# Optimization experiments

Measured on AMD Instinct MI355X. Metric: run time of the kernel, lower is better.

The kernel has to match this reference:

```python
import jax, jax.numpy as jnp
import numpy as np

N, M, F, B = 100000, 12, 64, 41  # atoms, max neighbors, atom feat dim, bond feat dim
EPS = 1e-5


def setup_inputs() -> dict:
    key = jax.random.key(0)
    ks = jax.random.split(key, 8)
    neighbor_indices = jax.random.randint(ks[0], (N, M), 0, N, dtype=jnp.int32)
    atom_features = jax.random.normal(ks[1], (N, F), dtype=jnp.float32)
    bond_features = jax.random.normal(ks[2], (N, M, B), dtype=jnp.float32)
    W = jax.random.normal(ks[3], (2 * F + B, 2 * F), dtype=jnp.float32) * 0.05
    b = jnp.zeros((2 * F,), dtype=jnp.float32)
    bn1_scale = 1.0 + 0.02 * jax.random.normal(ks[4], (2 * F,), dtype=jnp.float32)
    bn1_offset = 0.02 * jax.random.normal(ks[5], (2 * F,), dtype=jnp.float32)
    bn2_scale = 1.0 + 0.02 * jax.random.normal(ks[6], (F,), dtype=jnp.float32)
    bn2_offset = 0.02 * jax.random.normal(ks[7], (F,), dtype=jnp.float32)
    return {"neighbor_indices": neighbor_indices, "atom_features": atom_features,
            "bond_features": bond_features, "W": W, "b": b,
            "bn1_scale": bn1_scale, "bn1_offset": bn1_offset,
            "bn2_scale": bn2_scale, "bn2_offset": bn2_offset}


def batchnorm(x, scale, offset):
    # haiku BatchNorm, training mode: batch stats over all axes but channel (last)
    mean = jnp.mean(x, axis=0, keepdims=True)
    var = jnp.mean(jnp.square(x), axis=0, keepdims=True) - jnp.square(mean)
    inv = scale * jax.lax.rsqrt(var + EPS)
    return (x - mean) * inv + offset


def reference(neighbor_indices, atom_features, bond_features, W, b,
              bn1_scale, bn1_offset, bn2_scale, bn2_offset):
    n = atom_features.shape[0]
    nbr_feats = atom_features[neighbor_indices]  # (N, M, F) gather
    self_feats = jnp.broadcast_to(atom_features[:, None, :], (n, M, F))
    total = jnp.concatenate([self_feats, nbr_feats, bond_features], axis=2)  # (N, M, 2F+B)
    gated = total @ W + b  # (N, M, 2F)
    gated = batchnorm(gated.reshape(-1, 2 * F), bn1_scale, bn1_offset).reshape(n, M, 2 * F)
    nbr_filter, nbr_core = jnp.split(gated, 2, axis=2)
    summed = jnp.sum(jax.nn.sigmoid(nbr_filter) * jax.nn.softplus(nbr_core), axis=1)  # (N, F)
    summed = batchnorm(summed, bn2_scale, bn2_offset)
    return jax.nn.softplus(atom_features + summed)
```

## Files before the change

### kernel.cpp

```cpp
#include <hip/hip_runtime.h>
#include <hip/hip_bf16.h>
#include <math.h>


#define NATOMS  100000
#define MNBR    12
#define FDIM    64
#define BDIM    41
#define C2F     128
#define EPSBN   1e-5f
#define NBLK    2048
#define GROUPS  (NATOMS/4)
#define AR      136
#define PR      72

typedef __attribute__((ext_vector_type(8))) short  short8;
typedef __attribute__((ext_vector_type(4))) float  f32x4;

__device__ __forceinline__ float softplusf(float x) {
    return fmaxf(x, 0.f) + __logf(1.f + __expf(-fabsf(x)));
}
__device__ __forceinline__ float sigmoidf(float x) {
    return 1.f / (1.f + __expf(-x));
}
__device__ __forceinline__ unsigned short f2bf(float f) {
    unsigned int x = __builtin_bit_cast(unsigned int, f);
    unsigned int r = (x + 0x7fff + ((x >> 16) & 1)) >> 16;
    return (unsigned short)r;
}
__device__ __forceinline__ unsigned int pkbf(float a, float b) {
    unsigned short lo = __builtin_bit_cast(unsigned short, __float2bfloat16(a));
    unsigned short hi = __builtin_bit_cast(unsigned short, __float2bfloat16(b));
    return (unsigned)lo | ((unsigned)hi << 16);
}
__device__ __forceinline__ float bflo(unsigned int u) {
    return __builtin_bit_cast(float, u << 16);
}
__device__ __forceinline__ float bfhi(unsigned int u) {
    return __builtin_bit_cast(float, u & 0xffff0000u);
}
__device__ __forceinline__ float bf2f(unsigned short u) {
    return __builtin_bit_cast(float, ((unsigned int)u) << 16);
}

__global__ __launch_bounds__(256) void k_pack(
    const float* __restrict__ W,
    unsigned short* __restrict__ Wsn, unsigned short* __restrict__ Wpk)
{
    const int t0 = blockIdx.x*256 + threadIdx.x;
    for (int idx = t0; idx < 8*2*64*8; idx += gridDim.x*256) {
        int e = idx & 7, lane = (idx >> 3) & 63, ks = (idx >> 9) & 1, n = idx >> 10;
        int k   = ks*32 + (lane >> 4)*8 + e;
        int col = n*16 + (lane & 15);
        Wsn[idx] = f2bf(W[k*C2F + col]);
    }
    for (int idx = t0; idx < 8*4*64*8; idx += gridDim.x*256) {
        int e = idx & 7, lane = (idx >> 3) & 63, ks = (idx >> 9) & 3, n = idx >> 11;
        int k   = ks*32 + (lane >> 4)*8 + e;
        int col = n*16 + (lane & 15);
        float v = (k < 105) ? W[(64 + k)*C2F + col] : 0.f;
        Wpk[idx] = f2bf(v);
    }
}

__global__ __launch_bounds__(256, 4) void k_proj(
    const float* __restrict__ atomF, const unsigned short* __restrict__ Wsn,
    unsigned short* __restrict__ PselfBf)
{
    __shared__ __align__(16) unsigned short A[64*PR];
    const int tid = threadIdx.x, w = tid >> 6, lane = tid & 63;
    const int g = lane >> 4, x = lane & 15;
    short8 B0[2], B1[2];
    #pragma unroll
    for (int ks = 0; ks < 2; ++ks) {
        B0[ks] = *(const short8*)(Wsn + ((w*2 + ks)*64 + lane)*8);
        B1[ks] = *(const short8*)(Wsn + (((w+4)*2 + ks)*64 + lane)*8);
    }
    for (int a0 = blockIdx.x*64; a0 < NATOMS; a0 += gridDim.x*64) {
        __syncthreads();
        #pragma unroll
        for (int it = 0; it < 4; ++it) {
            int idx = it*256 + tid;
            int p = idx >> 4, c = idx & 15;
            int i = a0 + p;
            float4 v = make_float4(0.f, 0.f, 0.f, 0.f);
            if (i < NATOMS) v = *(const float4*)(atomF + (size_t)i*FDIM + 4*c);
            uint2 u; u.x = pkbf(v.x, v.y); u.y = pkbf(v.z, v.w);
            *(uint2*)(A + p*PR + 4*c) = u;
        }
        __syncthreads();
        f32x4 z = {0.f, 0.f, 0.f, 0.f};
        f32x4 acc[4][2];
        #pragma unroll
        for (int m = 0; m < 4; ++m) { acc[m][0] = z; acc[m][1] = z; }
        #pragma unroll
        for (int ks = 0; ks < 2; ++ks) {
            #pragma unroll
            for (int m = 0; m < 4; ++m) {
                short8 a = *(const short8*)(A + (m*16 + x)*PR + ks*32 + g*8);
                acc[m][0] = __builtin_amdgcn_mfma_f32_16x16x32_bf16(a, B0[ks], acc[m][0], 0, 0, 0);
                acc[m][1] = __builtin_amdgcn_mfma_f32_16x16x32_bf16(a, B1[ks], acc[m][1], 0, 0, 0);
            }
        }
        #pragma unroll
        for (int m = 0; m < 4; ++m) {
            int i = a0 + m*16 + g*4;
            #pragma unroll
            for (int rg = 0; rg < 4; ++rg) {
                if (i + rg < NATOMS) {
                    PselfBf[(size_t)(i+rg)*C2F + w*16 + x]     = f2bf(acc[m][0][rg]);
                    PselfBf[(size_t)(i+rg)*C2F + (w+4)*16 + x] = f2bf(acc[m][1][rg]);
                }
            }
        }
    }
}

__global__ __launch_bounds__(256, 4) void k_gemm(
    const int* __restrict__ nbr, const float* __restrict__ atomF,
    const float* __restrict__ bond, const unsigned short* __restrict__ Wpk,
    const unsigned short* __restrict__ PselfBf,
    uint4* __restrict__ gated, float* __restrict__ partial1)
{
    __shared__ __align__(16) unsigned short A[48*AR];
    __shared__ int Ni[48];
    const int tid = threadIdx.x, w = tid >> 6, lane = tid & 63;
    const int g = lane >> 4, x = lane & 15;
    const int ch0 = w*16 + x;
    short8 B0[4], B1[4];
    #pragma unroll
    for (int ks = 0; ks < 4; ++ks) {
        B0[ks] = *(const short8*)(Wpk + ((w*4 + ks)*64 + lane)*8);
        B1[ks] = *(const short8*)(Wpk + (((w+4)*4 + ks)*64 + lane)*8);
    }
    for (int idx = tid; idx < 48*AR/2; idx += 256) ((unsigned int*)A)[idx] = 0u;
    float s0 = 0.f, q0 = 0.f, s1 = 0.f, q1 = 0.f;

    for (int grp = blockIdx.x; grp < GROUPS; grp += gridDim.x) {
        const int base = grp*4;
        __syncthreads();
        if (tid < 48) Ni[tid] = nbr[base*MNBR + tid];
        __syncthreads();
        #pragma unroll
        for (int it = 0; it < 6; ++it) {
            int idx = it*256 + tid;
            int p = idx >> 5, c = idx & 31;
            if (c < 16) {
                int r = Ni[p];
                float4 v = *(const float4*)(atomF + (size_t)r*FDIM + 4*c);
                uint2 u; u.x = pkbf(v.x, v.y); u.y = pkbf(v.z, v.w);
                *(uint2*)(A + p*AR + 4*c) = u;
            } else if (c < 27) {
                int cc = c - 16;
                int pa = p/12;
                const float* bp = bond + (size_t)(base + pa)*(MNBR*BDIM)
                                       + (p - pa*12)*BDIM + 4*cc;
                float b0 = bp[0], b1 = 0.f, b2 = 0.f, b3 = 0.f;
                if (cc < 10) { b1 = bp[1]; b2 = bp[2]; b3 = bp[3]; }
                uint2 u; u.x = pkbf(b0, b1); u.y = pkbf(b2, b3);
                *(uint2*)(A + p*AR + 64 + 4*cc) = u;
            }
        }
        __syncthreads();
        f32x4 z = {0.f, 0.f, 0.f, 0.f};
        f32x4 acc[3][2];
        #pragma unroll
        for (int m = 0; m < 3; ++m) { acc[m][0] = z; acc[m][1] = z; }
        #pragma unroll
        for (int ks = 0; ks < 4; ++ks) {
            #pragma unroll
            for (int m = 0; m < 3; ++m) {
                short8 a = *(const short8*)(A + (m*16 + x)*AR + ks*32 + g*8);
                acc[m][0] = __builtin_amdgcn_mfma_f32_16x16x32_bf16(a, B0[ks], acc[m][0], 0, 0, 0);
                acc[m][1] = __builtin_amdgcn_mfma_f32_16x16x32_bf16(a, B1[ks], acc[m][1], 0, 0, 0);
            }
        }
        uint4* gbase = gated + ((size_t)grp*4 + w)*3*64 + lane;
        #pragma unroll
        for (int m = 0; m < 3; ++m) {
            int ia = base + (m*16 + g*4)/12;
            float ps0 = bf2f(PselfBf[(size_t)ia*C2F + ch0]);
            float ps1 = bf2f(PselfBf[(size_t)ia*C2F + 64 + ch0]);
            float v00 = acc[m][0][0] + ps0, v01 = acc[m][0][1] + ps0;
            float v02 = acc[m][0][2] + ps0, v03 = acc[m][0][3] + ps0;
            float v10 = acc[m][1][0] + ps1, v11 = acc[m][1][1] + ps1;
            float v12 = acc[m][1][2] + ps1, v13 = acc[m][1][3] + ps1;
            s0 += (v00 + v01) + (v02 + v03);
            s1 += (v10 + v11) + (v12 + v13);
            q0 = fmaf(v00, v00, q0); q0 = fmaf(v01, v01, q0);
            q0 = fmaf(v02, v02, q0); q0 = fmaf(v03, v03, q0);
            q1 = fmaf(v10, v10, q1); q1 = fmaf(v11, v11, q1);
            q1 = fmaf(v12, v12, q1); q1 = fmaf(v13, v13, q1);
            uint4 pk;
            pk.x = pkbf(v00, v01); pk.y = pkbf(v02, v03);
            pk.z = pkbf(v10, v11); pk.w = pkbf(v12, v13);
            gbase[m*64] = pk;
        }
    }
    s0 += __shfl_xor(s0, 16); s0 += __shfl_xor(s0, 32);
    s1 += __shfl_xor(s1, 16); s1 += __shfl_xor(s1, 32);
    q0 += __shfl_xor(q0, 16); q0 += __shfl_xor(q0, 32);
    q1 += __shfl_xor(q1, 16); q1 += __shfl_xor(q1, 32);
    if (g == 0) {
        float* pb = partial1 + blockIdx.x*256;
        pb[ch0]            = s0; pb[64 + ch0]        = s1;
        pb[C2F + ch0]      = q0; pb[C2F + 64 + ch0]  = q1;
    }
}

__global__ __launch_bounds__(256) void k_red(
    const float* __restrict__ in, float* __restrict__ outp, int width)
{
    const int b = blockIdx.x;
    for (int c = threadIdx.x; c < width; c += 256) {
        float s = 0.f;
        #pragma unroll 4
        for (int k = 0; k < 16; ++k) s += in[(size_t)(b*16 + k)*width + c];
        outp[(size_t)b*width + c] = s;
    }
}

__global__ __launch_bounds__(1024) void k_bn1_finalize(
    const float* __restrict__ red1, const float* __restrict__ scale,
    const float* __restrict__ offset, float* __restrict__ prm1)
{
    __shared__ float redS[1024], redQ[1024];
    const int tid = threadIdx.x, c = tid & 127, h = tid >> 7;
    float S = 0.f, Q = 0.f;
    for (int blk = h; blk < 128; blk += 8) {
        S += red1[blk*256 + c];
        Q += red1[blk*256 + 128 + c];
    }
    redS[tid] = S; redQ[tid] = Q;
    __syncthreads();
    if (tid < 128) {
        float Sa = 0.f, Qa = 0.f;
        #pragma unroll
        for (int hh = 0; hh < 8; ++hh) { Sa += redS[hh*128 + c]; Qa += redQ[hh*128 + c]; }
        const float invn = 1.f / (float)(NATOMS * MNBR);
        float mean = Sa * invn;
        float var  = Qa * invn - mean*mean;
        float inv  = scale[c] * rsqrtf(var + EPSBN);
        prm1[c]       = inv;
        prm1[128 + c] = offset[c] - mean*inv;
    }
}

__global__ __launch_bounds__(256, 8) void k_apply(
    const uint4* __restrict__ gated, const float* __restrict__ prm1,
    float* __restrict__ summed, float* __restrict__ partial2)
{
    __shared__ float Y[12*66];
    __shared__ float red[256];
    const int tid = threadIdx.x, w = tid >> 6, lane = tid & 63;
    const int g = lane >> 4, x = lane & 15;
    const int ch0 = w*16 + x;
    const float iv0 = prm1[ch0],      of0 = prm1[C2F + ch0];
    const float iv1 = prm1[64 + ch0], of1 = prm1[C2F + 64 + ch0];
    float s2 = 0.f, q2 = 0.f;

    for (int grp = blockIdx.x; grp < GROUPS; grp += gridDim.x) {
        __syncthreads();
        const uint4* gbase = gated + ((size_t)grp*4 + w)*3*64 + lane;
        #pragma unroll
        for (int m = 0; m < 3; ++m) {
            uint4 pk = gbase[m*64];
            float y00 = bflo(pk.x)*iv0 + of0, y01 = bfhi(pk.x)*iv0 + of0;
            float y02 = bflo(pk.y)*iv0 + of0, y03 = bfhi(pk.y)*iv0 + of0;
            float y10 = bflo(pk.z)*iv1 + of1, y11 = bfhi(pk.z)*iv1 + of1;
            float y12 = bflo(pk.w)*iv1 + of1, y13 = bfhi(pk.w)*iv1 + of1;
            float sY = sigmoidf(y00)*softplusf(y10) + sigmoidf(y01)*softplusf(y11)
                     + sigmoidf(y02)*softplusf(y12) + sigmoidf(y03)*softplusf(y13);
            Y[(m*4 + g)*66 + ch0] = sY;
        }
        __syncthreads();
        float sv = Y[(3*w)*66 + lane] + Y[(3*w + 1)*66 + lane] + Y[(3*w + 2)*66 + lane];
        summed[(size_t)(grp*4 + w)*FDIM + lane] = sv;
        s2 += sv; q2 = fmaf(sv, sv, q2);
    }
    red[tid] = s2; __syncthreads();
    if (tid < 64) partial2[blockIdx.x*128 + tid]
        = red[tid] + red[tid+64] + red[tid+128] + red[tid+192];
    __syncthreads();
    red[tid] = q2; __syncthreads();
    if (tid < 64) partial2[blockIdx.x*128 + 64 + tid]
        = red[tid] + red[tid+64] + red[tid+128] + red[tid+192];
}

__global__ __launch_bounds__(1024) void k_bn2_finalize(
    const float* __restrict__ red2, const float* __restrict__ scale,
    const float* __restrict__ offset, float* __restrict__ prm2)
{
    __shared__ float redS[1024], redQ[1024];
    const int tid = threadIdx.x, f = tid & 63, h = tid >> 6;
    float S = 0.f, Q = 0.f;
    for (int blk = h; blk < 128; blk += 16) {
        S += red2[blk*128 + f];
        Q += red2[blk*128 + 64 + f];
    }
    redS[tid] = S; redQ[tid] = Q;
    __syncthreads();
    if (tid < 64) {
        float Sa = 0.f, Qa = 0.f;
        #pragma unroll
        for (int hh = 0; hh < 16; ++hh) { Sa += redS[hh*64 + f]; Qa += redQ[hh*64 + f]; }
        const float invn = 1.f / (float)NATOMS;
        float mean = Sa * invn;
        float var  = Qa * invn - mean*mean;
        float inv  = scale[f] * rsqrtf(var + EPSBN);
        prm2[f]      = inv;
        prm2[64 + f] = offset[f] - mean*inv;
    }
}

__global__ __launch_bounds__(256) void k_final(
    const float* __restrict__ atomF, const float* __restrict__ summed,
    const float* __restrict__ prm2, float* __restrict__ out)
{
    __shared__ float iv[64], of[64];
    if (threadIdx.x < 64) {
        iv[threadIdx.x] = prm2[threadIdx.x];
        of[threadIdx.x] = prm2[64 + threadIdx.x];
    }
    __syncthreads();
    const int total4 = NATOMS*FDIM/4;
    for (int t = blockIdx.x*blockDim.x + threadIdx.x; t < total4;
         t += gridDim.x*blockDim.x) {
        float4 a = ((const float4*)atomF)[t];
        float4 s = ((const float4*)summed)[t];
        int fb = (t*4) & 63;
        float4 r;
        r.x = softplusf(a.x + s.x*iv[fb]   + of[fb]);
        r.y = softplusf(a.y + s.y*iv[fb+1] + of[fb+1]);
        r.z = softplusf(a.z + s.z*iv[fb+2] + of[fb+2]);
        r.w = softplusf(a.w + s.w*iv[fb+3] + of[fb+3]);
        ((float4*)out)[t] = r;
    }
}

extern "C" void kernel_launch(void* const* d_in, const int* in_sizes, int n_in,
                              void* d_out, int out_size, void* d_ws, size_t ws_size,
                              hipStream_t stream)
{
    const int*   nbr   = (const int*)  d_in[0];
    const float* atomF = (const float*)d_in[1];
    const float* bond  = (const float*)d_in[2];
    const float* W     = (const float*)d_in[3];
    const float* s1    = (const float*)d_in[5];
    const float* o1    = (const float*)d_in[6];
    const float* s2    = (const float*)d_in[7];
    const float* o2    = (const float*)d_in[8];
    float* out = (float*)d_out;

    uint4* gated        = (uint4*)d_ws;
    unsigned short* PselfBf = (unsigned short*)(gated + (size_t)GROUPS*12*64);
    float* summed   = (float*)(PselfBf + (size_t)NATOMS*C2F);
    float* partial1 = summed   + (size_t)NATOMS*FDIM;
    float* partial2 = partial1 + (size_t)NBLK*256;
    float* red1     = partial2 + (size_t)NBLK*128;
    float* red2     = red1     + 128*256;
    float* prm1     = red2     + 128*128;
    float* prm2     = prm1     + 256;
    unsigned short* Wsn = (unsigned short*)(prm2 + 128);
    unsigned short* Wpk = Wsn + 8192;

    hipLaunchKernelGGL(k_pack,         dim3(64),   dim3(256),  0, stream, W, Wsn, Wpk);
    hipLaunchKernelGGL(k_proj,         dim3(782),  dim3(256),  0, stream, atomF, Wsn, PselfBf);
    hipLaunchKernelGGL(k_gemm,         dim3(NBLK), dim3(256),  0, stream,
                       nbr, atomF, bond, Wpk, PselfBf, gated, partial1);
    hipLaunchKernelGGL(k_red,          dim3(128),  dim3(256),  0, stream, partial1, red1, 256);
    hipLaunchKernelGGL(k_bn1_finalize, dim3(1),    dim3(1024), 0, stream, red1, s1, o1, prm1);
    hipLaunchKernelGGL(k_apply,        dim3(NBLK), dim3(256),  0, stream,
                       gated, prm1, summed, partial2);
    hipLaunchKernelGGL(k_red,          dim3(128),  dim3(256),  0, stream, partial2, red2, 128);
    hipLaunchKernelGGL(k_bn2_finalize, dim3(1),    dim3(1024), 0, stream, red2, s2, o2, prm2);
    hipLaunchKernelGGL(k_final,        dim3(2048), dim3(256),  0, stream, atomF, summed, prm2, out);
}
```

Baseline: 397.3 us.

## Double-buffer neighbor tile loads and gather from a bf16 atom copy

k_proj now also writes a bf16 copy of the atom features, and k_gemm gathers neighbor rows from that copy, which halves the gather bytes. k_gemm's shared tile is double-buffered: the next group's gather and bond loads are issued into registers before the MFMA work on the current group and written to the alternate buffer afterward, which hides load latency. The Ni shared array and one barrier per iteration are dropped. The cost is extra registers for staging, twice the LDS, and an additional 12.8MB write in k_proj.

After: 394.2 us. No clear change (-0.8%).

```diff
diff --git a/kernel.cpp b/kernel.cpp
--- a/kernel.cpp
+++ b/kernel.cpp
@@ -65,7 +65,7 @@
 
 __global__ __launch_bounds__(256, 4) void k_proj(
     const float* __restrict__ atomF, const unsigned short* __restrict__ Wsn,
-    unsigned short* __restrict__ PselfBf)
+    unsigned short* __restrict__ PselfBf, unsigned short* __restrict__ atomBf)
 {
     __shared__ __align__(16) unsigned short A[64*PR];
     const int tid = threadIdx.x, w = tid >> 6, lane = tid & 63;
@@ -87,6 +87,7 @@
             if (i < NATOMS) v = *(const float4*)(atomF + (size_t)i*FDIM + 4*c);
             uint2 u; u.x = pkbf(v.x, v.y); u.y = pkbf(v.z, v.w);
             *(uint2*)(A + p*PR + 4*c) = u;
+            if (i < NATOMS) *(uint2*)(atomBf + (size_t)i*FDIM + 4*c) = u;
         }
         __syncthreads();
         f32x4 z = {0.f, 0.f, 0.f, 0.f};
@@ -117,13 +118,12 @@
 }
 
 __global__ __launch_bounds__(256, 4) void k_gemm(
-    const int* __restrict__ nbr, const float* __restrict__ atomF,
+    const int* __restrict__ nbr, const unsigned short* __restrict__ atomBf,
     const float* __restrict__ bond, const unsigned short* __restrict__ Wpk,
     const unsigned short* __restrict__ PselfBf,
     uint4* __restrict__ gated, float* __restrict__ partial1)
 {
-    __shared__ __align__(16) unsigned short A[48*AR];
-    __shared__ int Ni[48];
+    __shared__ __align__(16) unsigned short A[2][48*AR];
     const int tid = threadIdx.x, w = tid >> 6, lane = tid & 63;
     const int g = lane >> 4, x = lane & 15;
     const int ch0 = w*16 + x;
@@ -133,35 +133,47 @@
         B0[ks] = *(const short8*)(Wpk + ((w*4 + ks)*64 + lane)*8);
         B1[ks] = *(const short8*)(Wpk + (((w+4)*4 + ks)*64 + lane)*8);
     }
-    for (int idx = tid; idx < 48*AR/2; idx += 256) ((unsigned int*)A)[idx] = 0u;
+    for (int idx = tid; idx < 2*48*AR/2; idx += 256) ((unsigned int*)A)[idx] = 0u;
+
+    uint2 st[6];
     float s0 = 0.f, q0 = 0.f, s1 = 0.f, q1 = 0.f;
 
-    for (int grp = blockIdx.x; grp < GROUPS; grp += gridDim.x) {
-        const int base = grp*4;
-        __syncthreads();
-        if (tid < 48) Ni[tid] = nbr[base*MNBR + tid];
-        __syncthreads();
-        #pragma unroll
-        for (int it = 0; it < 6; ++it) {
-            int idx = it*256 + tid;
-            int p = idx >> 5, c = idx & 31;
-            if (c < 16) {
-                int r = Ni[p];
-                float4 v = *(const float4*)(atomF + (size_t)r*FDIM + 4*c);
-                uint2 u; u.x = pkbf(v.x, v.y); u.y = pkbf(v.z, v.w);
-                *(uint2*)(A + p*AR + 4*c) = u;
-            } else if (c < 27) {
-                int cc = c - 16;
-                int pa = p/12;
-                const float* bp = bond + (size_t)(base + pa)*(MNBR*BDIM)
-                                       + (p - pa*12)*BDIM + 4*cc;
-                float b0 = bp[0], b1 = 0.f, b2 = 0.f, b3 = 0.f;
-                if (cc < 10) { b1 = bp[1]; b2 = bp[2]; b3 = bp[3]; }
-                uint2 u; u.x = pkbf(b0, b1); u.y = pkbf(b2, b3);
-                *(uint2*)(A + p*AR + 64 + 4*cc) = u;
-            }
-        }
-        __syncthreads();
+#define LOADG(GRP)                                                            \
+    {   const int base_ = (GRP)*4;                                            \
+        _Pragma("unroll")                                                     \
+        for (int it = 0; it < 6; ++it) {                                      \
+            int idx = it*256 + tid;                                           \
+            int p = idx >> 5, c = idx & 31;                                   \
+            if (c < 16) {                                                     \
+                int r = nbr[base_*MNBR + p];                                  \
+                st[it] = *(const uint2*)(atomBf + ((size_t)r << 6) + 4*c);    \
+            } else if (c < 27) {                                              \
+                int cc = c - 16;                                              \
+                int pa = p/12;                                                \
+                const float* bp = bond + (size_t)(base_ + pa)*(MNBR*BDIM)     \
+                                       + (p - pa*12)*BDIM + 4*cc;             \
+                float b0 = bp[0], b1 = 0.f, b2 = 0.f, b3 = 0.f;               \
+                if (cc < 10) { b1 = bp[1]; b2 = bp[2]; b3 = bp[3]; }          \
+                st[it].x = pkbf(b0, b1); st[it].y = pkbf(b2, b3);             \
+            }                                                                 \
+        } }
+
+#define WRITEA(BUF)                                                           \
+    {   _Pragma("unroll")                                                     \
+        for (int it = 0; it < 6; ++it) {                                      \
+            int idx = it*256 + tid;                                           \
+            int p = idx >> 5, c = idx & 31;                                   \
+            if (c < 16)      *(uint2*)(&A[BUF][p*AR + 4*c]) = st[it];         \
+            else if (c < 27) *(uint2*)(&A[BUF][p*AR + 64 + 4*(c-16)]) = st[it]; \
+        } }
+
+    int grp = blockIdx.x;
+    int cur = 0;
+    if (grp < GROUPS) { LOADG(grp); WRITEA(0); }
+    for (; grp < GROUPS; grp += gridDim.x) {
+        const int nxt = grp + gridDim.x;
+        __syncthreads();
+        if (nxt < GROUPS) LOADG(nxt);
         f32x4 z = {0.f, 0.f, 0.f, 0.f};
         f32x4 acc[3][2];
         #pragma unroll
@@ -170,11 +182,12 @@
         for (int ks = 0; ks < 4; ++ks) {
             #pragma unroll
             for (int m = 0; m < 3; ++m) {
-                short8 a = *(const short8*)(A + (m*16 + x)*AR + ks*32 + g*8);
+                short8 a = *(const short8*)(&A[cur][(m*16 + x)*AR + ks*32 + g*8]);
                 acc[m][0] = __builtin_amdgcn_mfma_f32_16x16x32_bf16(a, B0[ks], acc[m][0], 0, 0, 0);
                 acc[m][1] = __builtin_amdgcn_mfma_f32_16x16x32_bf16(a, B1[ks], acc[m][1], 0, 0, 0);
             }
         }
+        const int base = grp*4;
         uint4* gbase = gated + ((size_t)grp*4 + w)*3*64 + lane;
         #pragma unroll
         for (int m = 0; m < 3; ++m) {
@@ -196,7 +209,11 @@
             pk.z = pkbf(v10, v11); pk.w = pkbf(v12, v13);
             gbase[m*64] = pk;
         }
-    }
+        if (nxt < GROUPS) WRITEA(cur ^ 1);
+        cur ^= 1;
+    }
+#undef LOADG
+#undef WRITEA
     s0 += __shfl_xor(s0, 16); s0 += __shfl_xor(s0, 32);
     s1 += __shfl_xor(s1, 16); s1 += __shfl_xor(s1, 32);
     q0 += __shfl_xor(q0, 16); q0 += __shfl_xor(q0, 32);
@@ -354,7 +371,8 @@
 
     uint4* gated        = (uint4*)d_ws;
     unsigned short* PselfBf = (unsigned short*)(gated + (size_t)GROUPS*12*64);
-    float* summed   = (float*)(PselfBf + (size_t)NATOMS*C2F);
+    unsigned short* atomBf  = PselfBf + (size_t)NATOMS*C2F;
+    float* summed   = (float*)(atomBf + (size_t)NATOMS*FDIM);
     float* partial1 = summed   + (size_t)NATOMS*FDIM;
     float* partial2 = partial1 + (size_t)NBLK*256;
     float* red1     = partial2 + (size_t)NBLK*128;
@@ -365,9 +383,10 @@
     unsigned short* Wpk = Wsn + 8192;
 
     hipLaunchKernelGGL(k_pack,         dim3(64),   dim3(256),  0, stream, W, Wsn, Wpk);
-    hipLaunchKernelGGL(k_proj,         dim3(782),  dim3(256),  0, stream, atomF, Wsn, PselfBf);
+    hipLaunchKernelGGL(k_proj,         dim3(782),  dim3(256),  0, stream,
+                       atomF, Wsn, PselfBf, atomBf);
     hipLaunchKernelGGL(k_gemm,         dim3(NBLK), dim3(256),  0, stream,
-                       nbr, atomF, bond, Wpk, PselfBf, gated, partial1);
+                       nbr, atomBf, bond, Wpk, PselfBf, gated, partial1);
     hipLaunchKernelGGL(k_red,          dim3(128),  dim3(256),  0, stream, partial1, red1, 256);
     hipLaunchKernelGGL(k_bn1_finalize, dim3(1),    dim3(1024), 0, stream, red1, s1, o1, prm1);
     hipLaunchKernelGGL(k_apply,        dim3(NBLK), dim3(256),  0, stream,
```

## Precompute neighbor projection per atom and gather projected rows instead of features

Applied to the files above, without the earlier changes.

The neighbor-feature part of the matmul is now computed once per atom in the projection kernel (atomF @ W_nbr, stored as bf16), alongside the self projection. The main kernel then only runs the bond-feature matmul (K reduced from 128 to 64) and adds gathered rows of the precomputed neighbor projection in its epilogue. This drops the per-edge gather-and-convert of 64 floats into shared memory and halves the MFMA work. In exchange, each gathered row is 128 bf16 values instead of 64 floats, projection output doubles in size, and the neighbor term gets an extra bf16 rounding. Occupancy hint raised to 6 and LDS row stride shrunk.

Result: slower. 492.4 us (+24.0%).

```diff
diff --git a/kernel.cpp b/kernel.cpp
--- a/kernel.cpp
+++ b/kernel.cpp
@@ -11,7 +11,7 @@
 #define EPSBN   1e-5f
 #define NBLK    2048
 #define GROUPS  (NATOMS/4)
-#define AR      136
+#define AR      72
 #define PR      72
 
 typedef __attribute__((ext_vector_type(8))) short  short8;
@@ -45,36 +45,39 @@
 
 __global__ __launch_bounds__(256) void k_pack(
     const float* __restrict__ W,
-    unsigned short* __restrict__ Wsn, unsigned short* __restrict__ Wpk)
+    unsigned short* __restrict__ Wal, unsigned short* __restrict__ Wbd)
 {
     const int t0 = blockIdx.x*256 + threadIdx.x;
+    for (int idx = t0; idx < 2*8*2*64*8; idx += gridDim.x*256) {
+        int e = idx & 7, lane = (idx >> 3) & 63, ks = (idx >> 9) & 1;
+        int n = (idx >> 10) & 7, h = idx >> 13;
+        int k   = h*64 + ks*32 + (lane >> 4)*8 + e;
+        int col = n*16 + (lane & 15);
+        Wal[idx] = f2bf(W[k*C2F + col]);
+    }
     for (int idx = t0; idx < 8*2*64*8; idx += gridDim.x*256) {
         int e = idx & 7, lane = (idx >> 3) & 63, ks = (idx >> 9) & 1, n = idx >> 10;
-        int k   = ks*32 + (lane >> 4)*8 + e;
+        int kk  = ks*32 + (lane >> 4)*8 + e;
         int col = n*16 + (lane & 15);
-        Wsn[idx] = f2bf(W[k*C2F + col]);
-    }
-    for (int idx = t0; idx < 8*4*64*8; idx += gridDim.x*256) {
-        int e = idx & 7, lane = (idx >> 3) & 63, ks = (idx >> 9) & 3, n = idx >> 11;
-        int k   = ks*32 + (lane >> 4)*8 + e;
-        int col = n*16 + (lane & 15);
-        float v = (k < 105) ? W[(64 + k)*C2F + col] : 0.f;
-        Wpk[idx] = f2bf(v);
+        float v = (kk < BDIM) ? W[(2*FDIM + kk)*C2F + col] : 0.f;
+        Wbd[idx] = f2bf(v);
     }
 }
 
 __global__ __launch_bounds__(256, 4) void k_proj(
-    const float* __restrict__ atomF, const unsigned short* __restrict__ Wsn,
-    unsigned short* __restrict__ PselfBf)
+    const float* __restrict__ atomF, const unsigned short* __restrict__ Wal,
+    unsigned short* __restrict__ PselfBf, unsigned short* __restrict__ PnbrBf)
 {
     __shared__ __align__(16) unsigned short A[64*PR];
     const int tid = threadIdx.x, w = tid >> 6, lane = tid & 63;
     const int g = lane >> 4, x = lane & 15;
-    short8 B0[2], B1[2];
+    short8 Bs0[2], Bs1[2], Bn0[2], Bn1[2];
     #pragma unroll
     for (int ks = 0; ks < 2; ++ks) {
-        B0[ks] = *(const short8*)(Wsn + ((w*2 + ks)*64 + lane)*8);
-        B1[ks] = *(const short8*)(Wsn + (((w+4)*2 + ks)*64 + lane)*8);
+        Bs0[ks] = *(const short8*)(Wal + (((0*8 + w    )*2 + ks)*64 + lane)*8);
+        Bs1[ks] = *(const short8*)(Wal + (((0*8 + w + 4)*2 + ks)*64 + lane)*8);
+        Bn0[ks] = *(const short8*)(Wal + (((1*8 + w    )*2 + ks)*64 + lane)*8);
+        Bn1[ks] = *(const short8*)(Wal + (((1*8 + w + 4)*2 + ks)*64 + lane)*8);
     }
     for (int a0 = blockIdx.x*64; a0 < NATOMS; a0 += gridDim.x*64) {
         __syncthreads();
@@ -90,16 +93,19 @@
         }
         __syncthreads();
         f32x4 z = {0.f, 0.f, 0.f, 0.f};
-        f32x4 acc[4][2];
-        #pragma unroll
-        for (int m = 0; m < 4; ++m) { acc[m][0] = z; acc[m][1] = z; }
+        f32x4 acc[4][4];
+        #pragma unroll
+        for (int m = 0; m < 4; ++m)
+            { acc[m][0] = z; acc[m][1] = z; acc[m][2] = z; acc[m][3] = z; }
         #pragma unroll
         for (int ks = 0; ks < 2; ++ks) {
             #pragma unroll
             for (int m = 0; m < 4; ++m) {
                 short8 a = *(const short8*)(A + (m*16 + x)*PR + ks*32 + g*8);
-                acc[m][0] = __builtin_amdgcn_mfma_f32_16x16x32_bf16(a, B0[ks], acc[m][0], 0, 0, 0);
-                acc[m][1] = __builtin_amdgcn_mfma_f32_16x16x32_bf16(a, B1[ks], acc[m][1], 0, 0, 0);
+                acc[m][0] = __builtin_amdgcn_mfma_f32_16x16x32_bf16(a, Bs0[ks], acc[m][0], 0, 0, 0);
+                acc[m][1] = __builtin_amdgcn_mfma_f32_16x16x32_bf16(a, Bs1[ks], acc[m][1], 0, 0, 0);
+                acc[m][2] = __builtin_amdgcn_mfma_f32_16x16x32_bf16(a, Bn0[ks], acc[m][2], 0, 0, 0);
+                acc[m][3] = __builtin_amdgcn_mfma_f32_16x16x32_bf16(a, Bn1[ks], acc[m][3], 0, 0, 0);
             }
         }
         #pragma unroll
@@ -108,30 +114,33 @@
             #pragma unroll
             for (int rg = 0; rg < 4; ++rg) {
                 if (i + rg < NATOMS) {
-                    PselfBf[(size_t)(i+rg)*C2F + w*16 + x]     = f2bf(acc[m][0][rg]);
-                    PselfBf[(size_t)(i+rg)*C2F + (w+4)*16 + x] = f2bf(acc[m][1][rg]);
+                    size_t o = (size_t)(i+rg)*C2F;
+                    PselfBf[o + w*16 + x]       = f2bf(acc[m][0][rg]);
+                    PselfBf[o + (w+4)*16 + x]   = f2bf(acc[m][1][rg]);
+                    PnbrBf [o + w*16 + x]       = f2bf(acc[m][2][rg]);
+                    PnbrBf [o + (w+4)*16 + x]   = f2bf(acc[m][3][rg]);
                 }
             }
         }
     }
 }
 
-__global__ __launch_bounds__(256, 4) void k_gemm(
-    const int* __restrict__ nbr, const float* __restrict__ atomF,
-    const float* __restrict__ bond, const unsigned short* __restrict__ Wpk,
+__global__ __launch_bounds__(256, 6) void k_gemm2(
+    const int* __restrict__ nbr, const float* __restrict__ bond,
+    const unsigned short* __restrict__ Wbd,
     const unsigned short* __restrict__ PselfBf,
+    const unsigned short* __restrict__ PnbrBf,
     uint4* __restrict__ gated, float* __restrict__ partial1)
 {
     __shared__ __align__(16) unsigned short A[48*AR];
-    __shared__ int Ni[48];
     const int tid = threadIdx.x, w = tid >> 6, lane = tid & 63;
     const int g = lane >> 4, x = lane & 15;
     const int ch0 = w*16 + x;
-    short8 B0[4], B1[4];
+    short8 B0[2], B1[2];
     #pragma unroll
-    for (int ks = 0; ks < 4; ++ks) {
-        B0[ks] = *(const short8*)(Wpk + ((w*4 + ks)*64 + lane)*8);
-        B1[ks] = *(const short8*)(Wpk + (((w+4)*4 + ks)*64 + lane)*8);
+    for (int ks = 0; ks < 2; ++ks) {
+        B0[ks] = *(const short8*)(Wbd + ((w*2 + ks)*64 + lane)*8);
+        B1[ks] = *(const short8*)(Wbd + (((w+4)*2 + ks)*64 + lane)*8);
     }
     for (int idx = tid; idx < 48*AR/2; idx += 256) ((unsigned int*)A)[idx] = 0u;
     float s0 = 0.f, q0 = 0.f, s1 = 0.f, q1 = 0.f;
@@ -139,26 +148,25 @@
     for (int grp = blockIdx.x; grp < GROUPS; grp += gridDim.x) {
         const int base = grp*4;
         __syncthreads();
-        if (tid < 48) Ni[tid] = nbr[base*MNBR + tid];
-        __syncthreads();
-        #pragma unroll
-        for (int it = 0; it < 6; ++it) {
+        int4 ridx[3];
+        float ps0[3], ps1[3];
+        #pragma unroll
+        for (int m = 0; m < 3; ++m) {
+            ridx[m] = *(const int4*)(nbr + base*MNBR + m*16 + g*4);
+            int ia = base + (m*16 + g*4)/12;
+            ps0[m] = bf2f(PselfBf[(size_t)ia*C2F + ch0]);
+            ps1[m] = bf2f(PselfBf[(size_t)ia*C2F + 64 + ch0]);
+        }
+        #pragma unroll
+        for (int it = 0; it < 3; ++it) {
             int idx = it*256 + tid;
-            int p = idx >> 5, c = idx & 31;
-            if (c < 16) {
-                int r = Ni[p];
-                float4 v = *(const float4*)(atomF + (size_t)r*FDIM + 4*c);
-                uint2 u; u.x = pkbf(v.x, v.y); u.y = pkbf(v.z, v.w);
-                *(uint2*)(A + p*AR + 4*c) = u;
-            } else if (c < 27) {
-                int cc = c - 16;
-                int pa = p/12;
-                const float* bp = bond + (size_t)(base + pa)*(MNBR*BDIM)
-                                       + (p - pa*12)*BDIM + 4*cc;
+            int p = idx >> 4, c = idx & 15;
+            if (c < 11) {
+                const float* bp = bond + (size_t)base*(MNBR*BDIM) + p*BDIM + 4*c;
                 float b0 = bp[0], b1 = 0.f, b2 = 0.f, b3 = 0.f;
-                if (cc < 10) { b1 = bp[1]; b2 = bp[2]; b3 = bp[3]; }
+                if (c < 10) { b1 = bp[1]; b2 = bp[2]; b3 = bp[3]; }
                 uint2 u; u.x = pkbf(b0, b1); u.y = pkbf(b2, b3);
-                *(uint2*)(A + p*AR + 64 + 4*cc) = u;
+                *(uint2*)(&A[p*AR + 4*c]) = u;
             }
         }
         __syncthreads();
@@ -167,10 +175,10 @@
         #pragma unroll
         for (int m = 0; m < 3; ++m) { acc[m][0] = z; acc[m][1] = z; }
         #pragma unroll
-        for (int ks = 0; ks < 4; ++ks) {
+        for (int ks = 0; ks < 2; ++ks) {
             #pragma unroll
             for (int m = 0; m < 3; ++m) {
-                short8 a = *(const short8*)(A + (m*16 + x)*AR + ks*32 + g*8);
+                short8 a = *(const short8*)(&A[(m*16 + x)*AR + ks*32 + g*8]);
                 acc[m][0] = __builtin_amdgcn_mfma_f32_16x16x32_bf16(a, B0[ks], acc[m][0], 0, 0, 0);
                 acc[m][1] = __builtin_amdgcn_mfma_f32_16x16x32_bf16(a, B1[ks], acc[m][1], 0, 0, 0);
             }
@@ -178,22 +186,19 @@
         uint4* gbase = gated + ((size_t)grp*4 + w)*3*64 + lane;
         #pragma unroll
         for (int m = 0; m < 3; ++m) {
-            int ia = base + (m*16 + g*4)/12;
-            float ps0 = bf2f(PselfBf[(size_t)ia*C2F + ch0]);
-            float ps1 = bf2f(PselfBf[(size_t)ia*C2F + 64 + ch0]);
-            float v00 = acc[m][0][0] + ps0, v01 = acc[m][0][1] + ps0;
-            float v02 = acc[m][0][2] + ps0, v03 = acc[m][0][3] + ps0;
-            float v10 = acc[m][1][0] + ps1, v11 = acc[m][1][1] + ps1;
-            float v12 = acc[m][1][2] + ps1, v13 = acc[m][1][3] + ps1;
-            s0 += (v00 + v01) + (v02 + v03);
-            s1 += (v10 + v11) + (v12 + v13);
-            q0 = fmaf(v00, v00, q0); q0 = fmaf(v01, v01, q0);
-            q0 = fmaf(v02, v02, q0); q0 = fmaf(v03, v03, q0);
-            q1 = fmaf(v10, v10, q1); q1 = fmaf(v11, v11, q1);
-            q1 = fmaf(v12, v12, q1); q1 = fmaf(v13, v13, q1);
+            const int rr[4] = {ridx[m].x, ridx[m].y, ridx[m].z, ridx[m].w};
+            float v0[4], v1[4];
+            #pragma unroll
+            for (int rg = 0; rg < 4; ++rg) {
+                size_t o = (size_t)rr[rg]*C2F;
+                v0[rg] = acc[m][0][rg] + ps0[m] + bf2f(PnbrBf[o + ch0]);
+                v1[rg] = acc[m][1][rg] + ps1[m] + bf2f(PnbrBf[o + 64 + ch0]);
+                s0 += v0[rg]; q0 = fmaf(v0[rg], v0[rg], q0);
+                s1 += v1[rg]; q1 = fmaf(v1[rg], v1[rg], q1);
+            }
             uint4 pk;
-            pk.x = pkbf(v00, v01); pk.y = pkbf(v02, v03);
-            pk.z = pkbf(v10, v11); pk.w = pkbf(v12, v13);
+            pk.x = pkbf(v0[0], v0[1]); pk.y = pkbf(v0[2], v0[3]);
+            pk.z = pkbf(v1[0], v1[1]); pk.w = pkbf(v1[2], v1[3]);
             gbase[m*64] = pk;
         }
     }
@@ -214,8 +219,8 @@
     const int b = blockIdx.x;
     for (int c = threadIdx.x; c < width; c += 256) {
         float s = 0.f;
-        #pragma unroll 4
-        for (int k = 0; k < 16; ++k) s += in[(size_t)(b*16 + k)*width + c];
+        #pragma unroll
+        for (int k = 0; k < NBLK/128; ++k) s += in[(size_t)(b*(NBLK/128) + k)*width + c];
         outp[(size_t)b*width + c] = s;
     }
 }
@@ -354,20 +359,22 @@
 
     uint4* gated        = (uint4*)d_ws;
     unsigned short* PselfBf = (unsigned short*)(gated + (size_t)GROUPS*12*64);
-    float* summed   = (float*)(PselfBf + (size_t)NATOMS*C2F);
+    unsigned short* PnbrBf  = PselfBf + (size_t)NATOMS*C2F;
+    float* summed   = (float*)(PnbrBf + (size_t)NATOMS*C2F);
     float* partial1 = summed   + (size_t)NATOMS*FDIM;
     float* partial2 = partial1 + (size_t)NBLK*256;
     float* red1     = partial2 + (size_t)NBLK*128;
     float* red2     = red1     + 128*256;
     float* prm1     = red2     + 128*128;
     float* prm2     = prm1     + 256;
-    unsigned short* Wsn = (unsigned short*)(prm2 + 128);
-    unsigned short* Wpk = Wsn + 8192;
-
-    hipLaunchKernelGGL(k_pack,         dim3(64),   dim3(256),  0, stream, W, Wsn, Wpk);
-    hipLaunchKernelGGL(k_proj,         dim3(782),  dim3(256),  0, stream, atomF, Wsn, PselfBf);
-    hipLaunchKernelGGL(k_gemm,         dim3(NBLK), dim3(256),  0, stream,
-                       nbr, atomF, bond, Wpk, PselfBf, gated, partial1);
+    unsigned short* Wal = (unsigned short*)(prm2 + 128);
+    unsigned short* Wbd = Wal + 16384;
+
+    hipLaunchKernelGGL(k_pack,         dim3(64),   dim3(256),  0, stream, W, Wal, Wbd);
+    hipLaunchKernelGGL(k_proj,         dim3(1024), dim3(256),  0, stream,
+                       atomF, Wal, PselfBf, PnbrBf);
+    hipLaunchKernelGGL(k_gemm2,        dim3(NBLK), dim3(256),  0, stream,
+                       nbr, bond, Wbd, PselfBf, PnbrBf, gated, partial1);
     hipLaunchKernelGGL(k_red,          dim3(128),  dim3(256),  0, stream, partial1, red1, 256);
     hipLaunchKernelGGL(k_bn1_finalize, dim3(1),    dim3(1024), 0, stream, red1, s1, o1, prm1);
     hipLaunchKernelGGL(k_apply,        dim3(NBLK), dim3(256),  0, stream,
```
